# Optimization experiments

Hardware: AMD Instinct MI355X
Metric: run time of the kernel (lower is better)

Reference implementation:

```python
import jax, jax.numpy as jnp
import numpy as np

B, S, H, K = 64, 512, 768, 64
NR, NN, ND = 9, 3, 3


def setup_inputs() -> dict:
    key = jax.random.key(0)
    ks = jax.random.split(key, 20)
    inp = {}
    inp["sequence_output"] = jax.random.normal(ks[0], (B, S, H), jnp.float32)
    for i, name in enumerate(["rel", "nov", "dir"]):
        inp[f"{name}_idx"] = jax.random.randint(ks[1 + i], (B, K), 0, S)
        inp[f"{name}_len"] = jax.random.randint(ks[4 + i], (B,), 0, K + 1)
    scale = 0.02
    for i, (name, nlab) in enumerate([("rel", NR), ("nov", NN), ("dir", ND)]):
        k0, k1 = jax.random.split(ks[7 + i])
        inp[f"{name}_dense_W"] = scale * jax.random.normal(k0, (H, H), jnp.float32)
        inp[f"{name}_dense_b"] = jnp.zeros((H,), jnp.float32)
        inp[f"{name}_cls_W"] = scale * jax.random.normal(k1, (nlab, H), jnp.float32)
        inp[f"{name}_cls_b"] = jnp.zeros((nlab,), jnp.float32)
    return inp


def _attn_pool(seq, idx, length):
    """Ragged intra-group self-attention pooling (get_token_reps / get_ne_reps).

    seq: [B,S,H]; idx: [B,K] padded token indices; length: [B] valid counts.
    Original computes (softmax(G G^T) @ G)[0]; only row 0 of the attention is
    needed, so we compute just that row.
    """
    G = jnp.take_along_axis(seq, idx[:, :, None], axis=1)  # [B,K,H]
    mask = jnp.arange(idx.shape[1])[None, :] < length[:, None]  # [B,K]
    scores0 = jnp.einsum('bh,bjh->bj', G[:, 0], G)  # row 0 of G G^T
    scores0 = jnp.where(mask, scores0, jnp.float32(-1e30))
    a0 = jax.nn.softmax(scores0, axis=-1)  # [B,K]
    pooled = jnp.einsum('bj,bjh->bh', a0, G)  # [B,H]
    # empty-group fallback: sequence_output[b, 0]
    return jnp.where(length[:, None] > 0, pooled, seq[:, 0])


def _head(rep, Wd, bd, Wc, bc):
    # HiddenTokenPooler dense + tanh, then token classifier
    h = jnp.tanh(rep @ Wd.T + bd)
    return h @ Wc.T + bc


def reference(sequence_output, rel_idx, rel_len, nov_idx, nov_len, dir_idx, dir_len,
              rel_dense_W, rel_dense_b, rel_cls_W, rel_cls_b,
              nov_dense_W, nov_dense_b, nov_cls_W, nov_cls_b,
              dir_dense_W, dir_dense_b, dir_cls_W, dir_cls_b):
    rel_rep = _attn_pool(sequence_output, rel_idx, rel_len)
    nov_rep = _attn_pool(sequence_output, nov_idx, nov_len)
    dir_rep = _attn_pool(sequence_output, dir_idx, dir_len)
    rel_logits = _head(rel_rep, rel_dense_W, rel_dense_b, rel_cls_W, rel_cls_b)
    nov_logits = _head(nov_rep, nov_dense_W, nov_dense_b, nov_cls_W, nov_cls_b)
    dir_logits = _head(dir_rep, dir_dense_W, dir_dense_b, dir_cls_W, dir_cls_b)
    return (rel_logits, nov_logits, dir_logits)
```

## Files before the change

kernel.cpp:

```cpp
#include <hip/hip_runtime.h>
#include <math.h>


#define Hdim 768
#define Kdim 64
#define Sdim 512
#define Bdim 64
#define LDK  72

typedef float f32x4 __attribute__((ext_vector_type(4)));
typedef short bf16x8 __attribute__((ext_vector_type(8)));

__device__ __forceinline__ float wave_sum(float v) {
#pragma unroll
    for (int off = 32; off > 0; off >>= 1) v += __shfl_down(v, off, 64);
    return v;
}

__device__ __forceinline__ unsigned short f2bf(float f) {
    union { float f; unsigned int u; } c; c.f = f;
    unsigned int u = c.u + 0x7FFFu + ((c.u >> 16) & 1u);
    return (unsigned short)(u >> 16);
}

__global__ __launch_bounds__(1024) void k_pool(
    const float* __restrict__ seq,
    const int* __restrict__ idxr, const int* __restrict__ lenr,
    const int* __restrict__ idxn, const int* __restrict__ lenn,
    const int* __restrict__ idxd, const int* __restrict__ lend,
    float* __restrict__ pooled)
{
    const int b = blockIdx.x, g = blockIdx.y;
    const int tid = threadIdx.x, lane = tid & 63, wave = tid >> 6;

    const int* idxp = (g == 0) ? idxr : (g == 1) ? idxn : idxd;
    const int* lnp  = (g == 0) ? lenr : (g == 1) ? lenn : lend;

    __shared__ int   sidx[Kdim];
    __shared__ float attn[Kdim];
    __shared__ float wpart[16 * Hdim];

    if (tid < Kdim) sidx[tid] = idxp[b * Kdim + tid];
    const int len = lnp[b];
    __syncthreads();

    {
        const float* row0 = seq + ((size_t)b * Sdim + sidx[0]) * Hdim;
        float g0[12];
#pragma unroll
        for (int k = 0; k < 3; ++k) {
            float4 v = *(const float4*)(row0 + 4 * lane + 256 * k);
            g0[4 * k + 0] = v.x; g0[4 * k + 1] = v.y;
            g0[4 * k + 2] = v.z; g0[4 * k + 3] = v.w;
        }
        for (int j = wave; j < len; j += 16) {
            const float* rowj = seq + ((size_t)b * Sdim + sidx[j]) * Hdim;
            float acc = 0.f;
#pragma unroll
            for (int k = 0; k < 3; ++k) {
                float4 v = *(const float4*)(rowj + 4 * lane + 256 * k);
                acc += g0[4 * k + 0] * v.x + g0[4 * k + 1] * v.y
                     + g0[4 * k + 2] * v.z + g0[4 * k + 3] * v.w;
            }
            acc = wave_sum(acc);
            if (lane == 0) attn[j] = acc;
        }
    }
    __syncthreads();

    if (wave == 0 && len > 0) {
        float s = (lane < len) ? attn[lane] : -1e30f;
        float mx = s;
#pragma unroll
        for (int off = 32; off > 0; off >>= 1) mx = fmaxf(mx, __shfl_xor(mx, off, 64));
        float e = (lane < len) ? __expf(s - mx) : 0.f;
        float sum = e;
#pragma unroll
        for (int off = 32; off > 0; off >>= 1) sum += __shfl_xor(sum, off, 64);
        attn[lane] = e / sum;
    }
    __syncthreads();

    float* dst = pooled + ((size_t)g * Bdim + b) * Hdim;
    if (len > 0) {
        float p[12] = {0,0,0,0,0,0,0,0,0,0,0,0};
        const int j1 = min(wave * 4 + 4, len);
        for (int j = wave * 4; j < j1; ++j) {
            float a = attn[j];
            const float* rowj = seq + ((size_t)b * Sdim + sidx[j]) * Hdim;
#pragma unroll
            for (int k = 0; k < 3; ++k) {
                float4 v = *(const float4*)(rowj + 4 * lane + 256 * k);
                p[4 * k + 0] += a * v.x; p[4 * k + 1] += a * v.y;
                p[4 * k + 2] += a * v.z; p[4 * k + 3] += a * v.w;
            }
        }
#pragma unroll
        for (int k = 0; k < 3; ++k)
            *(float4*)&wpart[wave * Hdim + 4 * lane + 256 * k] =
                make_float4(p[4 * k], p[4 * k + 1], p[4 * k + 2], p[4 * k + 3]);
        __syncthreads();
        if (tid < Hdim) {
            float acc = 0.f;
#pragma unroll
            for (int w = 0; w < 16; ++w) acc += wpart[w * Hdim + tid];
            dst[tid] = acc;
        }
    } else {
        if (tid < Hdim) dst[tid] = seq[(size_t)b * Sdim * Hdim + tid];
    }
}

__global__ __launch_bounds__(256) void k_dense(
    const float* __restrict__ pooled,
    const float* __restrict__ dWr, const float* __restrict__ dbr,
    const float* __restrict__ dWn, const float* __restrict__ dbn,
    const float* __restrict__ dWd, const float* __restrict__ dbd,
    float* __restrict__ hvecT)
{
    const int mt = blockIdx.x, g = blockIdx.y;
    const float* dW = (g == 0) ? dWr : (g == 1) ? dWn : dWd;
    const float* db = (g == 0) ? dbr : (g == 1) ? dbn : dbd;
    const int i0 = mt * 64;

    const int tid = threadIdx.x, lane = tid & 63, wv = tid >> 6;
    const int q = lane >> 4, col = lane & 15;

    __shared__ unsigned short Ws[64 * LDK];
    __shared__ unsigned short Ps[64 * LDK];

    f32x4 acc[4] = {{0,0,0,0},{0,0,0,0},{0,0,0,0},{0,0,0,0}};

    const int srow  = tid >> 2;
    const int cbase = (tid & 3) * 16;
    const float* Pg = pooled + (size_t)g * Bdim * Hdim;

    for (int kk = 0; kk < Hdim; kk += 64) {
#pragma unroll
        for (int u = 0; u < 4; ++u) {
            int c = cbase + 4 * u;
            float4 w4 = *(const float4*)(dW + (size_t)(i0 + srow) * Hdim + kk + c);
            float4 p4 = *(const float4*)(Pg + (size_t)srow * Hdim + kk + c);
            ushort4 wb = make_ushort4(f2bf(w4.x), f2bf(w4.y), f2bf(w4.z), f2bf(w4.w));
            ushort4 pb = make_ushort4(f2bf(p4.x), f2bf(p4.y), f2bf(p4.z), f2bf(p4.w));
            *(ushort4*)&Ws[srow * LDK + c] = wb;
            *(ushort4*)&Ps[srow * LDK + c] = pb;
        }
        __syncthreads();
#pragma unroll
        for (int ks = 0; ks < 64; ks += 32) {
            bf16x8 a = *(const bf16x8*)&Ws[(wv * 16 + col) * LDK + ks + 8 * q];
#pragma unroll
            for (int n = 0; n < 4; ++n) {
                bf16x8 bb = *(const bf16x8*)&Ps[(n * 16 + col) * LDK + ks + 8 * q];
                acc[n] = __builtin_amdgcn_mfma_f32_16x16x32_bf16(a, bb, acc[n], 0, 0, 0);
            }
        }
        __syncthreads();
    }

#pragma unroll
    for (int n = 0; n < 4; ++n) {
        int b = n * 16 + col;
#pragma unroll
        for (int r = 0; r < 4; ++r) {
            int i = i0 + wv * 16 + q * 4 + r;
            float v = tanhf(acc[n][r] + db[i]);
            hvecT[((size_t)g * Hdim + i) * Bdim + b] = v;
        }
    }
}

__global__ __launch_bounds__(256) void k_cls(
    const float* __restrict__ hvecT,
    const float* __restrict__ cWr, const float* __restrict__ cbr,
    const float* __restrict__ cWn, const float* __restrict__ cbn,
    const float* __restrict__ cWd, const float* __restrict__ cbd,
    float* __restrict__ out)
{
    const int id = blockIdx.x;
    int g, c, nlab, off;
    if (id < 9)       { g = 0; c = id;      nlab = 9; off = 0;   }
    else if (id < 12) { g = 1; c = id - 9;  nlab = 3; off = 576; }
    else              { g = 2; c = id - 12; nlab = 3; off = 768; }
    const float* cW = (g == 0) ? cWr : (g == 1) ? cWn : cWd;
    const float* cb = (g == 0) ? cbr : (g == 1) ? cbn : cbd;

    const int b = threadIdx.x & 63;
    const int chunk = threadIdx.x >> 6;
    const float* hT = hvecT + (size_t)g * Hdim * Bdim;
    const float* wr = cW + (size_t)c * Hdim;

    float acc = 0.f;
    const int ibase = chunk * 192;
#pragma unroll 16
    for (int i = ibase; i < ibase + 192; ++i)
        acc += wr[i] * hT[i * Bdim + b];

    __shared__ float red[4][Bdim];
    red[chunk][b] = acc;
    __syncthreads();
    if (chunk == 0)
        out[off + b * nlab + c] = red[0][b] + red[1][b] + red[2][b] + red[3][b] + cb[c];
}

extern "C" void kernel_launch(void* const* d_in, const int* in_sizes, int n_in,
                              void* d_out, int out_size, void* d_ws, size_t ws_size,
                              hipStream_t stream) {
    const float* seq  = (const float*)d_in[0];
    const int*   idxr = (const int*)d_in[1];
    const int*   lenr = (const int*)d_in[2];
    const int*   idxn = (const int*)d_in[3];
    const int*   lenn = (const int*)d_in[4];
    const int*   idxd = (const int*)d_in[5];
    const int*   lend = (const int*)d_in[6];
    const float* dWr  = (const float*)d_in[7];
    const float* dbr  = (const float*)d_in[8];
    const float* cWr  = (const float*)d_in[9];
    const float* cbr  = (const float*)d_in[10];
    const float* dWn  = (const float*)d_in[11];
    const float* dbn  = (const float*)d_in[12];
    const float* cWn  = (const float*)d_in[13];
    const float* cbn  = (const float*)d_in[14];
    const float* dWd  = (const float*)d_in[15];
    const float* dbd  = (const float*)d_in[16];
    const float* cWd  = (const float*)d_in[17];
    const float* cbd  = (const float*)d_in[18];
    float* out = (float*)d_out;

    float* pooled = (float*)d_ws;
    float* hvecT  = pooled + 3 * Bdim * Hdim;

    k_pool<<<dim3(Bdim, 3), 1024, 0, stream>>>(seq, idxr, lenr, idxn, lenn, idxd, lend, pooled);
    k_dense<<<dim3(Hdim / 64, 3), 256, 0, stream>>>(pooled, dWr, dbr, dWn, dbn, dWd, dbd, hvecT);
    k_cls<<<15, 256, 0, stream>>>(hvecT, cWr, cbr, cWn, cbn, cWd, cbd, out);
}
```

Baseline: 197.5 us.

## Use single-pass online softmax pooling and fuse classifier into dense kernel

```diff
diff --git a/kernel.cpp b/kernel.cpp
--- a/kernel.cpp
+++ b/kernel.cpp
@@ -11,12 +11,6 @@
 typedef float f32x4 __attribute__((ext_vector_type(4)));
 typedef short bf16x8 __attribute__((ext_vector_type(8)));
 
-__device__ __forceinline__ float wave_sum(float v) {
-#pragma unroll
-    for (int off = 32; off > 0; off >>= 1) v += __shfl_down(v, off, 64);
-    return v;
-}
-
 __device__ __forceinline__ unsigned short f2bf(float f) {
     union { float f; unsigned int u; } c; c.f = f;
     unsigned int u = c.u + 0x7FFFu + ((c.u >> 16) & 1u);
@@ -28,7 +22,10 @@
     const int* __restrict__ idxr, const int* __restrict__ lenr,
     const int* __restrict__ idxn, const int* __restrict__ lenn,
     const int* __restrict__ idxd, const int* __restrict__ lend,
-    float* __restrict__ pooled)
+    const float* __restrict__ cbr, const float* __restrict__ cbn,
+    const float* __restrict__ cbd,
+    float* __restrict__ pooled,
+    float* __restrict__ out)
 {
     const int b = blockIdx.x, g = blockIdx.y;
     const int tid = threadIdx.x, lane = tid & 63, wave = tid >> 6;
@@ -37,14 +34,22 @@
     const int* lnp  = (g == 0) ? lenr : (g == 1) ? lenn : lend;
 
     __shared__ int   sidx[Kdim];
-    __shared__ float attn[Kdim];
-    __shared__ float wpart[16 * Hdim];
+    __shared__ float wm[16], wl[16], coef[16];
+    __shared__ float wpart[16][Hdim];
 
     if (tid < Kdim) sidx[tid] = idxp[b * Kdim + tid];
     const int len = lnp[b];
+
+    if (b == 0) {
+        if (g == 0)      { if (tid < 576) out[tid]       = cbr[tid % 9]; }
+        else if (g == 1) { if (tid < 192) out[576 + tid] = cbn[tid % 3]; }
+        else             { if (tid < 192) out[768 + tid] = cbd[tid % 3]; }
+    }
     __syncthreads();
 
-    {
+    float* dst = pooled + ((size_t)g * Bdim + b) * Hdim;
+
+    if (len > 0) {
         const float* row0 = seq + ((size_t)b * Sdim + sidx[0]) * Hdim;
         float g0[12];
 #pragma unroll
@@ -53,57 +58,58 @@
             g0[4 * k + 0] = v.x; g0[4 * k + 1] = v.y;
             g0[4 * k + 2] = v.z; g0[4 * k + 3] = v.w;
         }
+
+        float m = -1e30f, l = 0.f;
+        float p[12] = {0,0,0,0,0,0,0,0,0,0,0,0};
+
         for (int j = wave; j < len; j += 16) {
             const float* rowj = seq + ((size_t)b * Sdim + sidx[j]) * Hdim;
-            float acc = 0.f;
+            float v[12];
 #pragma unroll
             for (int k = 0; k < 3; ++k) {
-                float4 v = *(const float4*)(rowj + 4 * lane + 256 * k);
-                acc += g0[4 * k + 0] * v.x + g0[4 * k + 1] * v.y
-                     + g0[4 * k + 2] * v.z + g0[4 * k + 3] * v.w;
+                float4 t = *(const float4*)(rowj + 4 * lane + 256 * k);
+                v[4 * k + 0] = t.x; v[4 * k + 1] = t.y;
+                v[4 * k + 2] = t.z; v[4 * k + 3] = t.w;
             }
-            acc = wave_sum(acc);
-            if (lane == 0) attn[j] = acc;
-        }
-    }
-    __syncthreads();
-
-    if (wave == 0 && len > 0) {
-        float s = (lane < len) ? attn[lane] : -1e30f;
-        float mx = s;
-#pragma unroll
-        for (int off = 32; off > 0; off >>= 1) mx = fmaxf(mx, __shfl_xor(mx, off, 64));
-        float e = (lane < len) ? __expf(s - mx) : 0.f;
-        float sum = e;
-#pragma unroll
-        for (int off = 32; off > 0; off >>= 1) sum += __shfl_xor(sum, off, 64);
-        attn[lane] = e / sum;
-    }
-    __syncthreads();
-
-    float* dst = pooled + ((size_t)g * Bdim + b) * Hdim;
-    if (len > 0) {
-        float p[12] = {0,0,0,0,0,0,0,0,0,0,0,0};
-        const int j1 = min(wave * 4 + 4, len);
-        for (int j = wave * 4; j < j1; ++j) {
-            float a = attn[j];
-            const float* rowj = seq + ((size_t)b * Sdim + sidx[j]) * Hdim;
-#pragma unroll
-            for (int k = 0; k < 3; ++k) {
-                float4 v = *(const float4*)(rowj + 4 * lane + 256 * k);
-                p[4 * k + 0] += a * v.x; p[4 * k + 1] += a * v.y;
-                p[4 * k + 2] += a * v.z; p[4 * k + 3] += a * v.w;
-            }
-        }
+            float s = 0.f;
+#pragma unroll
+            for (int k = 0; k < 12; ++k) s += g0[k] * v[k];
+#pragma unroll
+            for (int off = 32; off > 0; off >>= 1) s += __shfl_xor(s, off, 64);
+
+            float mn    = fmaxf(m, s);
+            float scale = __expf(m - mn);
+            float e     = __expf(s - mn);
+            l = l * scale + e;
+#pragma unroll
+            for (int k = 0; k < 12; ++k) p[k] = p[k] * scale + e * v[k];
+            m = mn;
+        }
+
+        if (lane == 0) { wm[wave] = m; wl[wave] = l; }
 #pragma unroll
         for (int k = 0; k < 3; ++k)
-            *(float4*)&wpart[wave * Hdim + 4 * lane + 256 * k] =
+            *(float4*)&wpart[wave][4 * lane + 256 * k] =
                 make_float4(p[4 * k], p[4 * k + 1], p[4 * k + 2], p[4 * k + 3]);
         __syncthreads();
+
+        if (wave == 0 && lane < 16) {
+            float mw = wm[lane], lw = wl[lane];
+            float M = mw;
+#pragma unroll
+            for (int off = 8; off > 0; off >>= 1) M = fmaxf(M, __shfl_xor(M, off, 64));
+            float sc = __expf(mw - M);
+            float Ls = lw * sc;
+#pragma unroll
+            for (int off = 8; off > 0; off >>= 1) Ls += __shfl_xor(Ls, off, 64);
+            coef[lane] = sc / Ls;
+        }
+        __syncthreads();
+
         if (tid < Hdim) {
             float acc = 0.f;
 #pragma unroll
-            for (int w = 0; w < 16; ++w) acc += wpart[w * Hdim + tid];
+            for (int w = 0; w < 16; ++w) acc += wpart[w][tid] * coef[w];
             dst[tid] = acc;
         }
     } else {
@@ -111,16 +117,21 @@
     }
 }
 
-__global__ __launch_bounds__(256) void k_dense(
+__global__ __launch_bounds__(256) void k_dense_cls(
     const float* __restrict__ pooled,
     const float* __restrict__ dWr, const float* __restrict__ dbr,
+    const float* __restrict__ cWr,
     const float* __restrict__ dWn, const float* __restrict__ dbn,
+    const float* __restrict__ cWn,
     const float* __restrict__ dWd, const float* __restrict__ dbd,
-    float* __restrict__ hvecT)
+    const float* __restrict__ cWd,
+    float* __restrict__ out)
 {
     const int mt = blockIdx.x, g = blockIdx.y;
-    const float* dW = (g == 0) ? dWr : (g == 1) ? dWn : dWd;
-    const float* db = (g == 0) ? dbr : (g == 1) ? dbn : dbd;
+    const float *dW, *db, *cW; int nlab, off;
+    if (g == 0)      { dW = dWr; db = dbr; cW = cWr; nlab = 9; off = 0;   }
+    else if (g == 1) { dW = dWn; db = dbn; cW = cWn; nlab = 3; off = 576; }
+    else             { dW = dWd; db = dbd; cW = cWd; nlab = 3; off = 768; }
     const int i0 = mt * 64;
 
     const int tid = threadIdx.x, lane = tid & 63, wv = tid >> 6;
@@ -128,6 +139,7 @@
 
     __shared__ unsigned short Ws[64 * LDK];
     __shared__ unsigned short Ps[64 * LDK];
+    __shared__ float hs[64][65];
 
     f32x4 acc[4] = {{0,0,0,0},{0,0,0,0},{0,0,0,0},{0,0,0,0}};
 
@@ -141,10 +153,8 @@
             int c = cbase + 4 * u;
             float4 w4 = *(const float4*)(dW + (size_t)(i0 + srow) * Hdim + kk + c);
             float4 p4 = *(const float4*)(Pg + (size_t)srow * Hdim + kk + c);
-            ushort4 wb = make_ushort4(f2bf(w4.x), f2bf(w4.y), f2bf(w4.z), f2bf(w4.w));
-            ushort4 pb = make_ushort4(f2bf(p4.x), f2bf(p4.y), f2bf(p4.z), f2bf(p4.w));
-            *(ushort4*)&Ws[srow * LDK + c] = wb;
-            *(ushort4*)&Ps[srow * LDK + c] = pb;
+            *(ushort4*)&Ws[srow * LDK + c] = make_ushort4(f2bf(w4.x), f2bf(w4.y), f2bf(w4.z), f2bf(w4.w));
+            *(ushort4*)&Ps[srow * LDK + c] = make_ushort4(f2bf(p4.x), f2bf(p4.y), f2bf(p4.z), f2bf(p4.w));
         }
         __syncthreads();
 #pragma unroll
@@ -161,47 +171,23 @@
 
 #pragma unroll
     for (int n = 0; n < 4; ++n) {
-        int b = n * 16 + col;
+        int bb = n * 16 + col;
 #pragma unroll
         for (int r = 0; r < 4; ++r) {
-            int i = i0 + wv * 16 + q * 4 + r;
-            float v = tanhf(acc[n][r] + db[i]);
-            hvecT[((size_t)g * Hdim + i) * Bdim + b] = v;
-        }
-    }
-}
-
-__global__ __launch_bounds__(256) void k_cls(
-    const float* __restrict__ hvecT,
-    const float* __restrict__ cWr, const float* __restrict__ cbr,
-    const float* __restrict__ cWn, const float* __restrict__ cbn,
-    const float* __restrict__ cWd, const float* __restrict__ cbd,
-    float* __restrict__ out)
-{
-    const int id = blockIdx.x;
-    int g, c, nlab, off;
-    if (id < 9)       { g = 0; c = id;      nlab = 9; off = 0;   }
-    else if (id < 12) { g = 1; c = id - 9;  nlab = 3; off = 576; }
-    else              { g = 2; c = id - 12; nlab = 3; off = 768; }
-    const float* cW = (g == 0) ? cWr : (g == 1) ? cWn : cWd;
-    const float* cb = (g == 0) ? cbr : (g == 1) ? cbn : cbd;
-
-    const int b = threadIdx.x & 63;
-    const int chunk = threadIdx.x >> 6;
-    const float* hT = hvecT + (size_t)g * Hdim * Bdim;
-    const float* wr = cW + (size_t)c * Hdim;
-
-    float acc = 0.f;
-    const int ibase = chunk * 192;
+            int il = wv * 16 + q * 4 + r;
+            hs[il][bb] = tanhf(acc[n][r] + db[i0 + il]);
+        }
+    }
+    __syncthreads();
+
+    for (int c = wv; c < nlab; c += 4) {
+        const float* wr = cW + (size_t)c * Hdim + i0;
+        float a = 0.f;
 #pragma unroll 16
-    for (int i = ibase; i < ibase + 192; ++i)
-        acc += wr[i] * hT[i * Bdim + b];
-
-    __shared__ float red[4][Bdim];
-    red[chunk][b] = acc;
-    __syncthreads();
-    if (chunk == 0)
-        out[off + b * nlab + c] = red[0][b] + red[1][b] + red[2][b] + red[3][b] + cb[c];
+        for (int il = 0; il < 64; ++il)
+            a += wr[il] * hs[il][lane];
+        atomicAdd(&out[off + lane * nlab + c], a);
+    }
 }
 
 extern "C" void kernel_launch(void* const* d_in, const int* in_sizes, int n_in,
@@ -229,9 +215,9 @@
     float* out = (float*)d_out;
 
     float* pooled = (float*)d_ws;
-    float* hvecT  = pooled + 3 * Bdim * Hdim;
-
-    k_pool<<<dim3(Bdim, 3), 1024, 0, stream>>>(seq, idxr, lenr, idxn, lenn, idxd, lend, pooled);
-    k_dense<<<dim3(Hdim / 64, 3), 256, 0, stream>>>(pooled, dWr, dbr, dWn, dbn, dWd, dbd, hvecT);
-    k_cls<<<15, 256, 0, stream>>>(hvecT, cWr, cbr, cWn, cbn, cWd, cbd, out);
-}
+
+    k_pool<<<dim3(Bdim, 3), 1024, 0, stream>>>(
+        seq, idxr, lenr, idxn, lenn, idxd, lend, cbr, cbn, cbd, pooled, out);
+    k_dense_cls<<<dim3(Hdim / 64, 3), 256, 0, stream>>>(
+        pooled, dWr, dbr, cWr, dWn, dbn, cWn, dWd, dbd, cWd, out);
+}
```

Result: faster. 189.1 us (-4.3%).
